# Kernel tuning notes

Measured on AMD Instinct MI355X. Metric: run time of the kernel, lower is better.

## Reference

```python
import jax, jax.numpy as jnp
import numpy as np

N_NODES = 50000
N_EDGES = 800000
C_IN, C_HID, C_OUT = 256, 128, 64


def gcn_conv(x, src, dst, deg_inv_sqrt, W, b, n_nodes):
    """PyG GCNConv with self-loops already folded into (src, dst, deg).

    out[j] = sum_{(i->j)} d_i^{-1/2} d_j^{-1/2} (x W)[i] + b
    """
    h = x @ W  # [N, out]
    norm = deg_inv_sqrt[src] * deg_inv_sqrt[dst]  # [E+N]
    msg = h[src] * norm[:, None]  # [E+N, out]
    out = jax.ops.segment_sum(msg, dst, num_segments=n_nodes)
    return out + b


def setup_inputs() -> dict:
    key = jax.random.key(0)
    k1, k2, k3, k4, k5, k6 = jax.random.split(key, 6)
    x = jax.random.normal(k1, (N_NODES, C_IN), dtype=jnp.float32)
    edge_index = jax.random.randint(k2, (2, N_EDGES), 0, N_NODES, dtype=jnp.int64)
    # Glorot-ish init for GCN weights
    W1 = jax.random.normal(k3, (C_IN, C_HID), dtype=jnp.float32) / np.sqrt(C_IN)
    b1 = jnp.zeros((C_HID,), dtype=jnp.float32)
    W2 = jax.random.normal(k4, (C_HID, C_OUT), dtype=jnp.float32) / np.sqrt(C_HID)
    b2 = jnp.zeros((C_OUT,), dtype=jnp.float32)
    return {"x": x, "edge_index": edge_index, "W1": W1, "b1": b1, "W2": W2, "b2": b2}


def reference(x, edge_index, W1, b1, W2, b2):
    n = x.shape[0]
    loop = jnp.arange(n, dtype=edge_index.dtype)
    src = jnp.concatenate([edge_index[0], loop])  # row (message source)
    dst = jnp.concatenate([edge_index[1], loop])  # col (aggregation target)
    # symmetric normalization degree: in-degree at dst, with self loops
    deg = jax.ops.segment_sum(jnp.ones_like(dst, dtype=x.dtype), dst, num_segments=n)
    deg_inv_sqrt = jnp.where(deg > 0, jax.lax.rsqrt(deg), 0.0)

    h = gcn_conv(x, src, dst, deg_inv_sqrt, W1, b1, n)
    h = jax.nn.relu(h)
    # Dropout is identity in eval mode (reference baseline is deterministic)
    out = gcn_conv(h, src, dst, deg_inv_sqrt, W2, b2, n)
    return out
```

## Files before the change

kernel.cpp:

```cpp
#include <hip/hip_runtime.h>


#define CIN 256
#define CHID 128
#define COUT 64
#define NSCAT 256

typedef unsigned short ushort_t;
typedef unsigned int uint_t;
typedef __attribute__((ext_vector_type(8))) short short8;
typedef __attribute__((ext_vector_type(4))) float f32x4;

__device__ inline ushort_t f2bf(float f) {
  union { float f; uint_t u; } v; v.f = f;
  uint_t r = v.u + 0x7FFFu + ((v.u >> 16) & 1u);
  return (ushort_t)(r >> 16);
}
__device__ inline float bf_lo(uint_t u) {
  union { uint_t u; float f; } v; v.u = u << 16;
  return v.f;
}
__device__ inline float bf_hi(uint_t u) {
  union { uint_t u; float f; } v; v.u = u & 0xFFFF0000u;
  return v.f;
}
__device__ inline uint_t pack2(float a, float b) {
  return (uint_t)f2bf(a) | ((uint_t)f2bf(b) << 16);
}

__global__ __launch_bounds__(256) void k_pre(const int* __restrict__ dst,
                                             int* __restrict__ cntmat,
                                             const float* __restrict__ W1,
                                             const float* __restrict__ W2,
                                             ushort_t* __restrict__ Wt1,
                                             ushort_t* __restrict__ Wt2,
                                             int e, int nbk) {
  const int tid = threadIdx.x;
  if (blockIdx.x < NSCAT) {
    __shared__ int h[256];
    h[tid] = 0;
    __syncthreads();
    const int per = (e + NSCAT - 1) / NSCAT;
    const int lo = blockIdx.x * per;
    const int hi = min(e, lo + per);
    for (int i = lo + tid; i < hi; i += 256) atomicAdd(&h[dst[i] >> 8], 1);
    __syncthreads();
    if (tid < nbk) cntmat[blockIdx.x * nbk + tid] = h[tid];
  } else {
    int i = (blockIdx.x - NSCAT) * 256 + tid;
    if (i < CIN * CHID) {
      int k = i % CIN, c = i / CIN;
      Wt1[i] = f2bf(W1[(size_t)k * CHID + c]);
    } else {
      int j = i - CIN * CHID;
      if (j < CHID * COUT) {
        int k = j % CHID, c = j / CHID;
        Wt2[j] = f2bf(W2[(size_t)k * COUT + c]);
      }
    }
  }
}

__global__ __launch_bounds__(256) void k_colscan(int* __restrict__ cntmat,
                                                 int* __restrict__ btot, int nbk) {
  __shared__ int s[NSCAT];
  const int k = blockIdx.x;
  const int tid = threadIdx.x;
  const int v = cntmat[tid * nbk + k];
  s[tid] = v;
  __syncthreads();
  for (int off = 1; off < NSCAT; off <<= 1) {
    int t = (tid >= off) ? s[tid - off] : 0;
    __syncthreads();
    s[tid] += t;
    __syncthreads();
  }
  cntmat[tid * nbk + k] = s[tid] - v;
  if (tid == NSCAT - 1) btot[k] = s[tid];
}

__global__ __launch_bounds__(256) void k_bscatter(const int* __restrict__ src,
                                                  const int* __restrict__ dst,
                                                  const int* __restrict__ cntmat,
                                                  const int* __restrict__ btot,
                                                  int* __restrict__ pairs,
                                                  int e, int nbk) {
  __shared__ int s[256];
  __shared__ int cur[256];
  const int tid = threadIdx.x;
  const int v = (tid < nbk) ? btot[tid] : 0;
  s[tid] = v;
  __syncthreads();
  for (int off = 1; off < 256; off <<= 1) {
    int t = (tid >= off) ? s[tid - off] : 0;
    __syncthreads();
    s[tid] += t;
    __syncthreads();
  }
  cur[tid] = (tid < nbk) ? (s[tid] - v + cntmat[blockIdx.x * nbk + tid]) : 0;
  __syncthreads();
  const int per = (e + NSCAT - 1) / NSCAT;
  const int lo = blockIdx.x * per;
  const int hi = min(e, lo + per);
  for (int i = lo + tid; i < hi; i += 256) {
    int d = dst[i];
    int off = atomicAdd(&cur[d >> 8], 1);
    pairs[off] = (src[i] << 8) | (d & 255);
  }
}

__global__ __launch_bounds__(256) void k_bbuild(const int* __restrict__ pairs,
                                                const int* __restrict__ btot,
                                                int* __restrict__ rowptr,
                                                float* __restrict__ dinv,
                                                ushort_t* __restrict__ csr,
                                                int n, int e, int nbk) {
  __shared__ int h[256];
  __shared__ int s[256];
  __shared__ int sbnd[2];
  const int tid = threadIdx.x;
  const int b = blockIdx.x;
  {
    const int v = (tid < nbk) ? btot[tid] : 0;
    s[tid] = v;
    __syncthreads();
    for (int off = 1; off < 256; off <<= 1) {
      int t = (tid >= off) ? s[tid - off] : 0;
      __syncthreads();
      s[tid] += t;
      __syncthreads();
    }
    if (tid == b) {
      sbnd[0] = s[tid] - v;
      sbnd[1] = s[tid];
    }
    __syncthreads();
  }
  const int lo = sbnd[0];
  const int hi = sbnd[1];
  h[tid] = 0;
  __syncthreads();
  for (int i = lo + tid; i < hi; i += 256) atomicAdd(&h[pairs[i] & 255], 1);
  __syncthreads();
  const int deg = h[tid];
  s[tid] = deg;
  __syncthreads();
  for (int off = 1; off < 256; off <<= 1) {
    int t = (tid >= off) ? s[tid - off] : 0;
    __syncthreads();
    s[tid] += t;
    __syncthreads();
  }
  const int excl = s[tid] - deg;
  const int node = (b << 8) + tid;
  if (node < n) {
    rowptr[node] = lo + excl;
    dinv[node] = rsqrtf((float)(deg + 1));
  }
  if (b == 0 && tid == 0) rowptr[n] = e;
  h[tid] = lo + excl;
  __syncthreads();
  for (int i = lo + tid; i < hi; i += 256) {
    int p = pairs[i];
    int slot = atomicAdd(&h[p & 255], 1);
    csr[slot] = (ushort_t)(((uint_t)p) >> 8);
  }
}

template <int K, int BN, bool XBF16>
__global__ __launch_bounds__(256) void k_gemm_mfma(
    const void* __restrict__ Xv, const ushort_t* __restrict__ Wt,
    const float* __restrict__ dinv, ushort_t* __restrict__ out, int M) {
  constexpr int BM = 128, BK = 32;
  constexpr int NSUB = BN / 16;
  constexpr int ASZ = BM * BK;
  constexpr int BSZ = BK * BN;
  constexpr int NCH = K / BK;
  constexpr int AITF = ASZ / 4 / 256;
  constexpr int AITB = ASZ / 8 / 256;
  constexpr int BIT = BSZ / 8 / 256;

  __shared__ ushort_t As[2][ASZ];
  __shared__ ushort_t Bs[2][BSZ];

  const int tid = threadIdx.x;
  const int lane = tid & 63;
  const int w = tid >> 6;
  const int row0 = blockIdx.x * BM;

  const float* Xf = (const float*)Xv;
  const ushort_t* Xb = (const ushort_t*)Xv;

  float4 arf[AITF];
  uint4 arb[AITB];
  uint4 brg[BIT];

  auto load_A = [&](int kc) {
    if constexpr (XBF16) {
#pragma unroll
      for (int i = 0; i < AITB; ++i) {
        int fi = i * 256 + tid;
        int r = fi >> 2, q = fi & 3;
        int gr = min(row0 + r, M - 1);
        arb[i] = *(const uint4*)(Xb + (size_t)gr * K + kc + q * 8);
      }
    } else {
#pragma unroll
      for (int i = 0; i < AITF; ++i) {
        int fi = i * 256 + tid;
        int r = fi >> 3, q = fi & 7;
        int gr = min(row0 + r, M - 1);
        arf[i] = *(const float4*)(Xf + (size_t)gr * K + kc + q * 4);
      }
    }
#pragma unroll
    for (int i = 0; i < BIT; ++i) {
      int g = i * 256 + tid;
      int nf = g >> 6, l = g & 63;
      int c = nf * 16 + (l & 15), k0 = (l >> 4) * 8;
      brg[i] = *(const uint4*)(Wt + (size_t)c * K + kc + k0);
    }
  };

  auto write_lds = [&](int buf) {
    if constexpr (XBF16) {
#pragma unroll
      for (int i = 0; i < AITB; ++i) {
        int fi = i * 256 + tid;
        int r = fi >> 2, q = fi & 3;
        int flat = (r >> 4) * 512 + ((r & 15) + 16 * q) * 8;
        *(uint4*)&As[buf][flat] = arb[i];
      }
    } else {
#pragma unroll
      for (int i = 0; i < AITF; ++i) {
        int fi = i * 256 + tid;
        int r = fi >> 3, q = fi & 7;
        int kb = q >> 1, ko = (q & 1) * 4;
        int flat = (r >> 4) * 512 + ((r & 15) + 16 * kb) * 8 + ko;
        uint2 p;
        p.x = pack2(arf[i].x, arf[i].y);
        p.y = pack2(arf[i].z, arf[i].w);
        *(uint2*)&As[buf][flat] = p;
      }
    }
#pragma unroll
    for (int i = 0; i < BIT; ++i) {
      int g = i * 256 + tid;
      int nf = g >> 6, l = g & 63;
      *(uint4*)&Bs[buf][nf * 512 + l * 8] = brg[i];
    }
  };

  f32x4 acc[2][NSUB];
#pragma unroll
  for (int mi = 0; mi < 2; ++mi)
#pragma unroll
    for (int ni = 0; ni < NSUB; ++ni)
      acc[mi][ni] = (f32x4){0.f, 0.f, 0.f, 0.f};

  load_A(0);
  write_lds(0);

#pragma unroll 1
  for (int ch = 0; ch < NCH; ++ch) {
    const int cur = ch & 1;
    __syncthreads();
    if (ch + 1 < NCH) load_A((ch + 1) * BK);

    short8 af[2];
#pragma unroll
    for (int mi = 0; mi < 2; ++mi)
      af[mi] = *(const short8*)&As[cur][(2 * w + mi) * 512 + lane * 8];
    short8 bf[NSUB];
#pragma unroll
    for (int ni = 0; ni < NSUB; ++ni)
      bf[ni] = *(const short8*)&Bs[cur][ni * 512 + lane * 8];

#pragma unroll
    for (int mi = 0; mi < 2; ++mi)
#pragma unroll
      for (int ni = 0; ni < NSUB; ++ni)
        acc[mi][ni] = __builtin_amdgcn_mfma_f32_16x16x32_bf16(
            af[mi], bf[ni], acc[mi][ni], 0, 0, 0);

    if (ch + 1 < NCH) write_lds(cur ^ 1);
  }

  const int qrow = (lane >> 4) * 4;
  const int col16 = lane & 15;
#pragma unroll
  for (int mi = 0; mi < 2; ++mi) {
    int rbase = row0 + w * 32 + mi * 16 + qrow;
#pragma unroll
    for (int v = 0; v < 4; ++v) {
      int row = rbase + v;
      if (row < M) {
        float dn = dinv[row];
#pragma unroll
        for (int ni = 0; ni < NSUB; ++ni)
          out[(size_t)row * BN + ni * 16 + col16] = f2bf(dn * acc[mi][ni][v]);
      }
    }
  }
}

__global__ __launch_bounds__(256) void k_aggw_h(
    const ushort_t* __restrict__ hh, const int* __restrict__ rowptr,
    const ushort_t* __restrict__ csr, const float* __restrict__ dinv,
    const float* __restrict__ bias, ushort_t* __restrict__ out, int n) {
  const int tid = threadIdx.x;
  const int node = blockIdx.x * 4 + (tid >> 6);
  if (node >= n) return;
  const int lane = tid & 63;
  const int q = lane & 15;
  const int eg = lane >> 4;

  float acc[8];
#pragma unroll
  for (int j = 0; j < 8; ++j) acc[j] = 0.0f;

  const int beg = rowptr[node];
  const int end = rowptr[node + 1];
  for (int k = beg + eg; k < end; k += 4) {
    int s = csr[k];
    uint4 u = *(const uint4*)&hh[(size_t)s * CHID + q * 8];
    acc[0] += bf_lo(u.x); acc[1] += bf_hi(u.x);
    acc[2] += bf_lo(u.y); acc[3] += bf_hi(u.y);
    acc[4] += bf_lo(u.z); acc[5] += bf_hi(u.z);
    acc[6] += bf_lo(u.w); acc[7] += bf_hi(u.w);
  }
#pragma unroll
  for (int j = 0; j < 8; ++j) {
    acc[j] += __shfl_xor(acc[j], 16);
    acc[j] += __shfl_xor(acc[j], 32);
  }
  if (eg == 0) {
    uint4 u = *(const uint4*)&hh[(size_t)node * CHID + q * 8];
    acc[0] += bf_lo(u.x); acc[1] += bf_hi(u.x);
    acc[2] += bf_lo(u.y); acc[3] += bf_hi(u.y);
    acc[4] += bf_lo(u.z); acc[5] += bf_hi(u.z);
    acc[6] += bf_lo(u.w); acc[7] += bf_hi(u.w);
    const float dn = dinv[node];
    float4 b0 = *(const float4*)&bias[q * 8];
    float4 b1 = *(const float4*)&bias[q * 8 + 4];
    float r[8];
    r[0] = dn * acc[0] + b0.x; r[1] = dn * acc[1] + b0.y;
    r[2] = dn * acc[2] + b0.z; r[3] = dn * acc[3] + b0.w;
    r[4] = dn * acc[4] + b1.x; r[5] = dn * acc[5] + b1.y;
    r[6] = dn * acc[6] + b1.z; r[7] = dn * acc[7] + b1.w;
#pragma unroll
    for (int j = 0; j < 8; ++j) r[j] = fmaxf(r[j], 0.0f);
    uint4 o;
    o.x = pack2(r[0], r[1]); o.y = pack2(r[2], r[3]);
    o.z = pack2(r[4], r[5]); o.w = pack2(r[6], r[7]);
    *(uint4*)&out[(size_t)node * CHID + q * 8] = o;
  }
}

__global__ __launch_bounds__(256) void k_aggw_o(
    const ushort_t* __restrict__ hh, const int* __restrict__ rowptr,
    const ushort_t* __restrict__ csr, const float* __restrict__ dinv,
    const float* __restrict__ bias, float* __restrict__ out, int n) {
  const int tid = threadIdx.x;
  const int node = blockIdx.x * 4 + (tid >> 6);
  if (node >= n) return;
  const int lane = tid & 63;
  const int q = lane & 7;
  const int eg = lane >> 3;

  float acc[8];
#pragma unroll
  for (int j = 0; j < 8; ++j) acc[j] = 0.0f;

  const int beg = rowptr[node];
  const int end = rowptr[node + 1];
  for (int k = beg + eg; k < end; k += 8) {
    int s = csr[k];
    uint4 u = *(const uint4*)&hh[(size_t)s * COUT + q * 8];
    acc[0] += bf_lo(u.x); acc[1] += bf_hi(u.x);
    acc[2] += bf_lo(u.y); acc[3] += bf_hi(u.y);
    acc[4] += bf_lo(u.z); acc[5] += bf_hi(u.z);
    acc[6] += bf_lo(u.w); acc[7] += bf_hi(u.w);
  }
#pragma unroll
  for (int j = 0; j < 8; ++j) {
    acc[j] += __shfl_xor(acc[j], 8);
    acc[j] += __shfl_xor(acc[j], 16);
    acc[j] += __shfl_xor(acc[j], 32);
  }
  if (eg == 0) {
    uint4 u = *(const uint4*)&hh[(size_t)node * COUT + q * 8];
    acc[0] += bf_lo(u.x); acc[1] += bf_hi(u.x);
    acc[2] += bf_lo(u.y); acc[3] += bf_hi(u.y);
    acc[4] += bf_lo(u.z); acc[5] += bf_hi(u.z);
    acc[6] += bf_lo(u.w); acc[7] += bf_hi(u.w);
    const float dn = dinv[node];
    float4 b0 = *(const float4*)&bias[q * 8];
    float4 b1 = *(const float4*)&bias[q * 8 + 4];
    float4 o0, o1;
    o0.x = dn * acc[0] + b0.x; o0.y = dn * acc[1] + b0.y;
    o0.z = dn * acc[2] + b0.z; o0.w = dn * acc[3] + b0.w;
    o1.x = dn * acc[4] + b1.x; o1.y = dn * acc[5] + b1.y;
    o1.z = dn * acc[6] + b1.z; o1.w = dn * acc[7] + b1.w;
    *(float4*)&out[(size_t)node * COUT + q * 8] = o0;
    *(float4*)&out[(size_t)node * COUT + q * 8 + 4] = o1;
  }
}

extern "C" void kernel_launch(void* const* d_in, const int* in_sizes, int n_in,
                              void* d_out, int out_size, void* d_ws, size_t ws_size,
                              hipStream_t stream) {
  const float* x  = (const float*)d_in[0];
  const int*   ei = (const int*)d_in[1];
  const float* W1 = (const float*)d_in[2];
  const float* b1 = (const float*)d_in[3];
  const float* W2 = (const float*)d_in[4];
  const float* b2 = (const float*)d_in[5];
  float* out = (float*)d_out;

  const int n = in_sizes[0] / CIN;
  const int e = in_sizes[1] / 2;
  const int* src = ei;
  const int* dst = ei + e;
  const int nbk = (n + 255) >> 8;

  size_t off = 0;
  auto alloc = [&](size_t bytes) {
    size_t o = off;
    off = (off + bytes + 255) & ~(size_t)255;
    return o;
  };
  char* ws = (char*)d_ws;
  int*      cntmat = (int*)(ws + alloc((size_t)NSCAT * 256 * 4));
  int*      btot   = (int*)(ws + alloc(256 * 4));
  int*      rowptr = (int*)(ws + alloc((size_t)(n + 1) * 4));
  float*    dinv   = (float*)(ws + alloc((size_t)n * 4));
  ushort_t* csr    = (ushort_t*)(ws + alloc((size_t)e * 2));
  int*      pairs  = (int*)(ws + alloc((size_t)e * 4));
  ushort_t* wt1    = (ushort_t*)(ws + alloc((size_t)CIN * CHID * 2));
  ushort_t* wt2    = (ushort_t*)(ws + alloc((size_t)CHID * COUT * 2));
  ushort_t* hhA    = (ushort_t*)(ws + alloc((size_t)n * CHID * 2));
  ushort_t* hhB    = (ushort_t*)(ws + alloc((size_t)n * CHID * 2));

  const int WTB = (CIN * CHID + CHID * COUT + 255) / 256;

  k_pre<<<NSCAT + WTB, 256, 0, stream>>>(dst, cntmat, W1, W2, wt1, wt2, e, nbk);
  k_colscan<<<nbk, NSCAT, 0, stream>>>(cntmat, btot, nbk);
  k_bscatter<<<NSCAT, 256, 0, stream>>>(src, dst, cntmat, btot, pairs, e, nbk);
  k_bbuild<<<nbk, 256, 0, stream>>>(pairs, btot, rowptr, dinv, csr, n, e, nbk);

  k_gemm_mfma<CIN, CHID, false><<<(n + 127) / 128, 256, 0, stream>>>(
      x, wt1, dinv, hhA, n);
  k_aggw_h<<<(n + 3) / 4, 256, 0, stream>>>(hhA, rowptr, csr, dinv, b1, hhB, n);

  k_gemm_mfma<CHID, COUT, true><<<(n + 127) / 128, 256, 0, stream>>>(
      hhB, wt2, dinv, hhA, n);
  k_aggw_o<<<(n + 3) / 4, 256, 0, stream>>>(hhA, rowptr, csr, dinv, b2, out, n);
}
```

Before: 128.0 us.

## Overlap layer-1 GEMM with CSR build by moving dinv scaling into aggregation

The source-side dinv scaling moves out of the GEMM epilogue into the aggregation loops, applied per gathered neighbor with an FMA. With that dependency gone, the first GEMM no longer has to wait for the degree and CSR build. Its tiles are split across the scatter and build kernels as extra blocks, and the layer-1 GEMM launch is removed, so dense MFMA work can overlap the irregular sort and build work. The cost is an extra dinv gather per edge in both aggregations, and larger shared-memory use in the scatter and build blocks, which may lower their occupancy.

```diff
diff --git a/kernel.cpp b/kernel.cpp
--- a/kernel.cpp
+++ b/kernel.cpp
@@ -26,6 +26,144 @@
 }
 __device__ inline uint_t pack2(float a, float b) {
   return (uint_t)f2bf(a) | ((uint_t)f2bf(b) << 16);
+}
+
+template <int K, int BN, bool XBF16>
+__device__ inline void gemm_tile(int bid, const void* __restrict__ Xv,
+                                 const ushort_t* __restrict__ Wt,
+                                 ushort_t* __restrict__ out, int M,
+                                 ushort_t* __restrict__ smem) {
+  constexpr int BM = 128, BK = 32;
+  constexpr int NSUB = BN / 16;
+  constexpr int ASZ = BM * BK;
+  constexpr int BSZ = BK * BN;
+  constexpr int NCH = K / BK;
+  constexpr int AITF = ASZ / 4 / 256;
+  constexpr int AITB = ASZ / 8 / 256;
+  constexpr int BIT = BSZ / 8 / 256;
+
+  ushort_t* As[2] = {smem, smem + ASZ};
+  ushort_t* Bs[2] = {smem + 2 * ASZ, smem + 2 * ASZ + BSZ};
+
+  const int tid = threadIdx.x;
+  const int lane = tid & 63;
+  const int w = tid >> 6;
+  const int row0 = bid * BM;
+
+  const float* Xf = (const float*)Xv;
+  const ushort_t* Xb = (const ushort_t*)Xv;
+
+  float4 arf[AITF];
+  uint4 arb[AITB];
+  uint4 brg[BIT];
+
+  auto load_A = [&](int kc) {
+    if constexpr (XBF16) {
+#pragma unroll
+      for (int i = 0; i < AITB; ++i) {
+        int fi = i * 256 + tid;
+        int r = fi >> 2, q = fi & 3;
+        int gr = min(row0 + r, M - 1);
+        arb[i] = *(const uint4*)(Xb + (size_t)gr * K + kc + q * 8);
+      }
+    } else {
+#pragma unroll
+      for (int i = 0; i < AITF; ++i) {
+        int fi = i * 256 + tid;
+        int r = fi >> 3, q = fi & 7;
+        int gr = min(row0 + r, M - 1);
+        arf[i] = *(const float4*)(Xf + (size_t)gr * K + kc + q * 4);
+      }
+    }
+#pragma unroll
+    for (int i = 0; i < BIT; ++i) {
+      int g = i * 256 + tid;
+      int nf = g >> 6, l = g & 63;
+      int c = nf * 16 + (l & 15), k0 = (l >> 4) * 8;
+      brg[i] = *(const uint4*)(Wt + (size_t)c * K + kc + k0);
+    }
+  };
+
+  auto write_lds = [&](int buf) {
+    if constexpr (XBF16) {
+#pragma unroll
+      for (int i = 0; i < AITB; ++i) {
+        int fi = i * 256 + tid;
+        int r = fi >> 2, q = fi & 3;
+        int flat = (r >> 4) * 512 + ((r & 15) + 16 * q) * 8;
+        *(uint4*)&As[buf][flat] = arb[i];
+      }
+    } else {
+#pragma unroll
+      for (int i = 0; i < AITF; ++i) {
+        int fi = i * 256 + tid;
+        int r = fi >> 3, q = fi & 7;
+        int kb = q >> 1, ko = (q & 1) * 4;
+        int flat = (r >> 4) * 512 + ((r & 15) + 16 * kb) * 8 + ko;
+        uint2 p;
+        p.x = pack2(arf[i].x, arf[i].y);
+        p.y = pack2(arf[i].z, arf[i].w);
+        *(uint2*)&As[buf][flat] = p;
+      }
+    }
+#pragma unroll
+    for (int i = 0; i < BIT; ++i) {
+      int g = i * 256 + tid;
+      int nf = g >> 6, l = g & 63;
+      *(uint4*)&Bs[buf][nf * 512 + l * 8] = brg[i];
+    }
+  };
+
+  f32x4 acc[2][NSUB];
+#pragma unroll
+  for (int mi = 0; mi < 2; ++mi)
+#pragma unroll
+    for (int ni = 0; ni < NSUB; ++ni)
+      acc[mi][ni] = (f32x4){0.f, 0.f, 0.f, 0.f};
+
+  load_A(0);
+  write_lds(0);
+
+#pragma unroll 1
+  for (int ch = 0; ch < NCH; ++ch) {
+    const int cur = ch & 1;
+    __syncthreads();
+    if (ch + 1 < NCH) load_A((ch + 1) * BK);
+
+    short8 af[2];
+#pragma unroll
+    for (int mi = 0; mi < 2; ++mi)
+      af[mi] = *(const short8*)&As[cur][(2 * w + mi) * 512 + lane * 8];
+    short8 bf[NSUB];
+#pragma unroll
+    for (int ni = 0; ni < NSUB; ++ni)
+      bf[ni] = *(const short8*)&Bs[cur][ni * 512 + lane * 8];
+
+#pragma unroll
+    for (int mi = 0; mi < 2; ++mi)
+#pragma unroll
+      for (int ni = 0; ni < NSUB; ++ni)
+        acc[mi][ni] = __builtin_amdgcn_mfma_f32_16x16x32_bf16(
+            af[mi], bf[ni], acc[mi][ni], 0, 0, 0);
+
+    if (ch + 1 < NCH) write_lds(cur ^ 1);
+  }
+
+  const int qrow = (lane >> 4) * 4;
+  const int col16 = lane & 15;
+#pragma unroll
+  for (int mi = 0; mi < 2; ++mi) {
+    int rbase = row0 + w * 32 + mi * 16 + qrow;
+#pragma unroll
+    for (int v = 0; v < 4; ++v) {
+      int row = rbase + v;
+      if (row < M) {
+#pragma unroll
+        for (int ni = 0; ni < NSUB; ++ni)
+          out[(size_t)row * BN + ni * 16 + col16] = f2bf(acc[mi][ni][v]);
+      }
+    }
+  }
 }
 
 __global__ __launch_bounds__(256) void k_pre(const int* __restrict__ dst,
@@ -79,15 +217,20 @@
   if (tid == NSCAT - 1) btot[k] = s[tid];
 }
 
-__global__ __launch_bounds__(256) void k_bscatter(const int* __restrict__ src,
-                                                  const int* __restrict__ dst,
-                                                  const int* __restrict__ cntmat,
-                                                  const int* __restrict__ btot,
-                                                  int* __restrict__ pairs,
-                                                  int e, int nbk) {
-  __shared__ int s[256];
-  __shared__ int cur[256];
-  const int tid = threadIdx.x;
+__global__ __launch_bounds__(256) void k_scat_gemm1(
+    const int* __restrict__ src, const int* __restrict__ dst,
+    const int* __restrict__ cntmat, const int* __restrict__ btot,
+    int* __restrict__ pairs, int e, int nbk,
+    const float* __restrict__ X, const ushort_t* __restrict__ Wt1,
+    ushort_t* __restrict__ hh, int M) {
+  __shared__ ushort_t smem[16384];
+  const int tid = threadIdx.x;
+  if ((int)blockIdx.x >= NSCAT) {
+    gemm_tile<CIN, CHID, false>(blockIdx.x - NSCAT, X, Wt1, hh, M, smem);
+    return;
+  }
+  int* s = (int*)smem;
+  int* cur = s + 256;
   const int v = (tid < nbk) ? btot[tid] : 0;
   s[tid] = v;
   __syncthreads();
@@ -109,16 +252,21 @@
   }
 }
 
-__global__ __launch_bounds__(256) void k_bbuild(const int* __restrict__ pairs,
-                                                const int* __restrict__ btot,
-                                                int* __restrict__ rowptr,
-                                                float* __restrict__ dinv,
-                                                ushort_t* __restrict__ csr,
-                                                int n, int e, int nbk) {
-  __shared__ int h[256];
-  __shared__ int s[256];
-  __shared__ int sbnd[2];
-  const int tid = threadIdx.x;
+__global__ __launch_bounds__(256) void k_build_gemm1(
+    const int* __restrict__ pairs, const int* __restrict__ btot,
+    int* __restrict__ rowptr, float* __restrict__ dinv,
+    ushort_t* __restrict__ csr, int n, int e, int nbk,
+    const float* __restrict__ X, const ushort_t* __restrict__ Wt1,
+    ushort_t* __restrict__ hh, int M, int nt_a) {
+  __shared__ ushort_t smem[16384];
+  const int tid = threadIdx.x;
+  if ((int)blockIdx.x >= nbk) {
+    gemm_tile<CIN, CHID, false>(nt_a + blockIdx.x - nbk, X, Wt1, hh, M, smem);
+    return;
+  }
+  int* h = (int*)smem;
+  int* s = h + 256;
+  int* sbnd = s + 256;
   const int b = blockIdx.x;
   {
     const int v = (tid < nbk) ? btot[tid] : 0;
@@ -167,142 +315,11 @@
   }
 }
 
-template <int K, int BN, bool XBF16>
-__global__ __launch_bounds__(256) void k_gemm_mfma(
-    const void* __restrict__ Xv, const ushort_t* __restrict__ Wt,
-    const float* __restrict__ dinv, ushort_t* __restrict__ out, int M) {
-  constexpr int BM = 128, BK = 32;
-  constexpr int NSUB = BN / 16;
-  constexpr int ASZ = BM * BK;
-  constexpr int BSZ = BK * BN;
-  constexpr int NCH = K / BK;
-  constexpr int AITF = ASZ / 4 / 256;
-  constexpr int AITB = ASZ / 8 / 256;
-  constexpr int BIT = BSZ / 8 / 256;
-
-  __shared__ ushort_t As[2][ASZ];
-  __shared__ ushort_t Bs[2][BSZ];
-
-  const int tid = threadIdx.x;
-  const int lane = tid & 63;
-  const int w = tid >> 6;
-  const int row0 = blockIdx.x * BM;
-
-  const float* Xf = (const float*)Xv;
-  const ushort_t* Xb = (const ushort_t*)Xv;
-
-  float4 arf[AITF];
-  uint4 arb[AITB];
-  uint4 brg[BIT];
-
-  auto load_A = [&](int kc) {
-    if constexpr (XBF16) {
-#pragma unroll
-      for (int i = 0; i < AITB; ++i) {
-        int fi = i * 256 + tid;
-        int r = fi >> 2, q = fi & 3;
-        int gr = min(row0 + r, M - 1);
-        arb[i] = *(const uint4*)(Xb + (size_t)gr * K + kc + q * 8);
-      }
-    } else {
-#pragma unroll
-      for (int i = 0; i < AITF; ++i) {
-        int fi = i * 256 + tid;
-        int r = fi >> 3, q = fi & 7;
-        int gr = min(row0 + r, M - 1);
-        arf[i] = *(const float4*)(Xf + (size_t)gr * K + kc + q * 4);
-      }
-    }
-#pragma unroll
-    for (int i = 0; i < BIT; ++i) {
-      int g = i * 256 + tid;
-      int nf = g >> 6, l = g & 63;
-      int c = nf * 16 + (l & 15), k0 = (l >> 4) * 8;
-      brg[i] = *(const uint4*)(Wt + (size_t)c * K + kc + k0);
-    }
-  };
-
-  auto write_lds = [&](int buf) {
-    if constexpr (XBF16) {
-#pragma unroll
-      for (int i = 0; i < AITB; ++i) {
-        int fi = i * 256 + tid;
-        int r = fi >> 2, q = fi & 3;
-        int flat = (r >> 4) * 512 + ((r & 15) + 16 * q) * 8;
-        *(uint4*)&As[buf][flat] = arb[i];
-      }
-    } else {
-#pragma unroll
-      for (int i = 0; i < AITF; ++i) {
-        int fi = i * 256 + tid;
-        int r = fi >> 3, q = fi & 7;
-        int kb = q >> 1, ko = (q & 1) * 4;
-        int flat = (r >> 4) * 512 + ((r & 15) + 16 * kb) * 8 + ko;
-        uint2 p;
-        p.x = pack2(arf[i].x, arf[i].y);
-        p.y = pack2(arf[i].z, arf[i].w);
-        *(uint2*)&As[buf][flat] = p;
-      }
-    }
-#pragma unroll
-    for (int i = 0; i < BIT; ++i) {
-      int g = i * 256 + tid;
-      int nf = g >> 6, l = g & 63;
-      *(uint4*)&Bs[buf][nf * 512 + l * 8] = brg[i];
-    }
-  };
-
-  f32x4 acc[2][NSUB];
-#pragma unroll
-  for (int mi = 0; mi < 2; ++mi)
-#pragma unroll
-    for (int ni = 0; ni < NSUB; ++ni)
-      acc[mi][ni] = (f32x4){0.f, 0.f, 0.f, 0.f};
-
-  load_A(0);
-  write_lds(0);
-
-#pragma unroll 1
-  for (int ch = 0; ch < NCH; ++ch) {
-    const int cur = ch & 1;
-    __syncthreads();
-    if (ch + 1 < NCH) load_A((ch + 1) * BK);
-
-    short8 af[2];
-#pragma unroll
-    for (int mi = 0; mi < 2; ++mi)
-      af[mi] = *(const short8*)&As[cur][(2 * w + mi) * 512 + lane * 8];
-    short8 bf[NSUB];
-#pragma unroll
-    for (int ni = 0; ni < NSUB; ++ni)
-      bf[ni] = *(const short8*)&Bs[cur][ni * 512 + lane * 8];
-
-#pragma unroll
-    for (int mi = 0; mi < 2; ++mi)
-#pragma unroll
-      for (int ni = 0; ni < NSUB; ++ni)
-        acc[mi][ni] = __builtin_amdgcn_mfma_f32_16x16x32_bf16(
-            af[mi], bf[ni], acc[mi][ni], 0, 0, 0);
-
-    if (ch + 1 < NCH) write_lds(cur ^ 1);
-  }
-
-  const int qrow = (lane >> 4) * 4;
-  const int col16 = lane & 15;
-#pragma unroll
-  for (int mi = 0; mi < 2; ++mi) {
-    int rbase = row0 + w * 32 + mi * 16 + qrow;
-#pragma unroll
-    for (int v = 0; v < 4; ++v) {
-      int row = rbase + v;
-      if (row < M) {
-        float dn = dinv[row];
-#pragma unroll
-        for (int ni = 0; ni < NSUB; ++ni)
-          out[(size_t)row * BN + ni * 16 + col16] = f2bf(dn * acc[mi][ni][v]);
-      }
-    }
-  }
+__global__ __launch_bounds__(256) void k_gemm2(const ushort_t* __restrict__ X,
+                                               const ushort_t* __restrict__ Wt2,
+                                               ushort_t* __restrict__ out, int M) {
+  __shared__ ushort_t smem[12288];
+  gemm_tile<CHID, COUT, true>(blockIdx.x, X, Wt2, out, M, smem);
 }
 
 __global__ __launch_bounds__(256) void k_aggw_h(
@@ -324,11 +341,12 @@
   const int end = rowptr[node + 1];
   for (int k = beg + eg; k < end; k += 4) {
     int s = csr[k];
+    float ds = dinv[s];
     uint4 u = *(const uint4*)&hh[(size_t)s * CHID + q * 8];
-    acc[0] += bf_lo(u.x); acc[1] += bf_hi(u.x);
-    acc[2] += bf_lo(u.y); acc[3] += bf_hi(u.y);
-    acc[4] += bf_lo(u.z); acc[5] += bf_hi(u.z);
-    acc[6] += bf_lo(u.w); acc[7] += bf_hi(u.w);
+    acc[0] = fmaf(bf_lo(u.x), ds, acc[0]); acc[1] = fmaf(bf_hi(u.x), ds, acc[1]);
+    acc[2] = fmaf(bf_lo(u.y), ds, acc[2]); acc[3] = fmaf(bf_hi(u.y), ds, acc[3]);
+    acc[4] = fmaf(bf_lo(u.z), ds, acc[4]); acc[5] = fmaf(bf_hi(u.z), ds, acc[5]);
+    acc[6] = fmaf(bf_lo(u.w), ds, acc[6]); acc[7] = fmaf(bf_hi(u.w), ds, acc[7]);
   }
 #pragma unroll
   for (int j = 0; j < 8; ++j) {
@@ -336,12 +354,12 @@
     acc[j] += __shfl_xor(acc[j], 32);
   }
   if (eg == 0) {
+    const float dn = dinv[node];
     uint4 u = *(const uint4*)&hh[(size_t)node * CHID + q * 8];
-    acc[0] += bf_lo(u.x); acc[1] += bf_hi(u.x);
-    acc[2] += bf_lo(u.y); acc[3] += bf_hi(u.y);
-    acc[4] += bf_lo(u.z); acc[5] += bf_hi(u.z);
-    acc[6] += bf_lo(u.w); acc[7] += bf_hi(u.w);
-    const float dn = dinv[node];
+    acc[0] = fmaf(bf_lo(u.x), dn, acc[0]); acc[1] = fmaf(bf_hi(u.x), dn, acc[1]);
+    acc[2] = fmaf(bf_lo(u.y), dn, acc[2]); acc[3] = fmaf(bf_hi(u.y), dn, acc[3]);
+    acc[4] = fmaf(bf_lo(u.z), dn, acc[4]); acc[5] = fmaf(bf_hi(u.z), dn, acc[5]);
+    acc[6] = fmaf(bf_lo(u.w), dn, acc[6]); acc[7] = fmaf(bf_hi(u.w), dn, acc[7]);
     float4 b0 = *(const float4*)&bias[q * 8];
     float4 b1 = *(const float4*)&bias[q * 8 + 4];
     float r[8];
@@ -377,11 +395,12 @@
   const int end = rowptr[node + 1];
   for (int k = beg + eg; k < end; k += 8) {
     int s = csr[k];
+    float ds = dinv[s];
     uint4 u = *(const uint4*)&hh[(size_t)s * COUT + q * 8];
-    acc[0] += bf_lo(u.x); acc[1] += bf_hi(u.x);
-    acc[2] += bf_lo(u.y); acc[3] += bf_hi(u.y);
-    acc[4] += bf_lo(u.z); acc[5] += bf_hi(u.z);
-    acc[6] += bf_lo(u.w); acc[7] += bf_hi(u.w);
+    acc[0] = fmaf(bf_lo(u.x), ds, acc[0]); acc[1] = fmaf(bf_hi(u.x), ds, acc[1]);
+    acc[2] = fmaf(bf_lo(u.y), ds, acc[2]); acc[3] = fmaf(bf_hi(u.y), ds, acc[3]);
+    acc[4] = fmaf(bf_lo(u.z), ds, acc[4]); acc[5] = fmaf(bf_hi(u.z), ds, acc[5]);
+    acc[6] = fmaf(bf_lo(u.w), ds, acc[6]); acc[7] = fmaf(bf_hi(u.w), ds, acc[7]);
   }
 #pragma unroll
   for (int j = 0; j < 8; ++j) {
@@ -390,12 +409,12 @@
     acc[j] += __shfl_xor(acc[j], 32);
   }
   if (eg == 0) {
+    const float dn = dinv[node];
     uint4 u = *(const uint4*)&hh[(size_t)node * COUT + q * 8];
-    acc[0] += bf_lo(u.x); acc[1] += bf_hi(u.x);
-    acc[2] += bf_lo(u.y); acc[3] += bf_hi(u.y);
-    acc[4] += bf_lo(u.z); acc[5] += bf_hi(u.z);
-    acc[6] += bf_lo(u.w); acc[7] += bf_hi(u.w);
-    const float dn = dinv[node];
+    acc[0] = fmaf(bf_lo(u.x), dn, acc[0]); acc[1] = fmaf(bf_hi(u.x), dn, acc[1]);
+    acc[2] = fmaf(bf_lo(u.y), dn, acc[2]); acc[3] = fmaf(bf_hi(u.y), dn, acc[3]);
+    acc[4] = fmaf(bf_lo(u.z), dn, acc[4]); acc[5] = fmaf(bf_hi(u.z), dn, acc[5]);
+    acc[6] = fmaf(bf_lo(u.w), dn, acc[6]); acc[7] = fmaf(bf_hi(u.w), dn, acc[7]);
     float4 b0 = *(const float4*)&bias[q * 8];
     float4 b1 = *(const float4*)&bias[q * 8 + 4];
     float4 o0, o1;
@@ -424,6 +443,8 @@
   const int* src = ei;
   const int* dst = ei + e;
   const int nbk = (n + 255) >> 8;
+  const int nt1 = (n + 127) / 128;
+  const int nt1a = nt1 / 2;
 
   size_t off = 0;
   auto alloc = [&](size_t bytes) {
@@ -447,14 +468,11 @@
 
   k_pre<<<NSCAT + WTB, 256, 0, stream>>>(dst, cntmat, W1, W2, wt1, wt2, e, nbk);
   k_colscan<<<nbk, NSCAT, 0, stream>>>(cntmat, btot, nbk);
-  k_bscatter<<<NSCAT, 256, 0, stream>>>(src, dst, cntmat, btot, pairs, e, nbk);
-  k_bbuild<<<nbk, 256, 0, stream>>>(pairs, btot, rowptr, dinv, csr, n, e, nbk);
-
-  k_gemm_mfma<CIN, CHID, false><<<(n + 127) / 128, 256, 0, stream>>>(
-      x, wt1, dinv, hhA, n);
+  k_scat_gemm1<<<NSCAT + nt1a, 256, 0, stream>>>(
+      src, dst, cntmat, btot, pairs, e, nbk, x, wt1, hhA, n);
+  k_build_gemm1<<<nbk + (nt1 - nt1a), 256, 0, stream>>>(
+      pairs, btot, rowptr, dinv, csr, n, e, nbk, x, wt1, hhA, n, nt1a);
   k_aggw_h<<<(n + 3) / 4, 256, 0, stream>>>(hhA, rowptr, csr, dinv, b1, hhB, n);
-
-  k_gemm_mfma<CHID, COUT, true><<<(n + 127) / 128, 256, 0, stream>>>(
-      hhB, wt2, dinv, hhA, n);
+  k_gemm2<<<nt1, 256, 0, stream>>>(hhB, wt2, hhA, n);
   k_aggw_o<<<(n + 3) / 4, 256, 0, stream>>>(hhA, rowptr, csr, dinv, b2, out, n);
 }
```

New measurement: 137.3 us. 7.3% more time.
